# Kernel optimization log

Hardware: AMD Instinct MI355X
Metric: run time of the kernel (lower is better)

## Reference

```python
import jax, jax.numpy as jnp
import numpy as np

D_IN = 1024
D_OUT = 1024
NUM_HEADS = 16
HEAD_DIM = D_OUT // NUM_HEADS


def setup_inputs() -> dict:
    key = jax.random.key(0)
    k1, k2, k3, k4 = jax.random.split(key, 4)
    x = jax.random.normal(k1, (2, 2048, D_IN), dtype=jnp.float32)
    # Linear weights stored torch-style [out_features, in_features]
    W_qkv = jax.random.normal(k2, (3 * D_OUT, D_IN), dtype=jnp.float32) * (1.0 / np.sqrt(D_IN))
    W_out = jax.random.normal(k3, (D_OUT, D_OUT), dtype=jnp.float32) * (1.0 / np.sqrt(D_OUT))
    b_out = jax.random.normal(k4, (D_OUT,), dtype=jnp.float32) * 0.01
    return {"x": x, "W_qkv": W_qkv, "W_out": W_out, "b_out": b_out}


def reference(x, W_qkv, W_out, b_out):
    b, s, _ = x.shape
    qkv = jnp.einsum('bsi,oi->bso', x, W_qkv)  # [b, s, 3*d_out]
    q, k, v = jnp.split(qkv, 3, axis=-1)
    def to_heads(t):
        return t.reshape(b, s, NUM_HEADS, HEAD_DIM).transpose(0, 2, 1, 3)
    q, k, v = to_heads(q), to_heads(k), to_heads(v)
    # NOTE: original module does NOT scale by 1/sqrt(head_dim)
    scores = jnp.einsum('bhqd,bhkd->bhqk', q, k)
    causal = jnp.tril(jnp.ones((s, s), dtype=bool))  # True = keep
    scores = jnp.where(causal[None, None], scores, -jnp.inf)
    attn = jax.nn.softmax(scores, axis=-1)
    ctx = jnp.einsum('bhqk,bhkd->bhqd', attn, v)
    ctx = ctx.transpose(0, 2, 1, 3).reshape(b, s, D_OUT)
    return jnp.einsum('bso,po->bsp', ctx, W_out) + b_out
```

## Files before the change

kernel.cpp:

```cpp
#include <hip/hip_runtime.h>
#include <cstdint>
#include <cstddef>


typedef __attribute__((ext_vector_type(8))) short bf16x8;
typedef __attribute__((ext_vector_type(4))) float f32x4;

#define LOG2E 1.44269504f

#define MFMA16(a, b, c) __builtin_amdgcn_mfma_f32_16x16x32_bf16((a), (b), (c), 0, 0, 0)

#define GLDS16(g, s)                                                        \
  __builtin_amdgcn_global_load_lds(                                         \
      (const __attribute__((address_space(1))) void*)(g),                   \
      (__attribute__((address_space(3))) void*)(s), 16, 0, 0)

#if __has_builtin(__builtin_amdgcn_exp2f)
#define EXP2F(x) __builtin_amdgcn_exp2f(x)
#else
#define EXP2F(x) exp2f(x)
#endif

static __device__ __forceinline__ unsigned short f2bf(float f) {
  unsigned int u = __builtin_bit_cast(unsigned int, f);
  u += 0x7FFFu + ((u >> 16) & 1u);
  return (unsigned short)(u >> 16);
}

static __device__ __forceinline__ unsigned int pk2bf(float a, float b) {
  const unsigned int ua = __builtin_bit_cast(unsigned int, a) + 0x8000u;
  const unsigned int ub = __builtin_bit_cast(unsigned int, b) + 0x8000u;
  return __builtin_amdgcn_perm(ub, ua, 0x07060302);
}

__global__ __launch_bounds__(256) void cast_bf16(const float* __restrict__ x,
                                                 const float* __restrict__ wq,
                                                 const float* __restrict__ wo,
                                                 unsigned short* __restrict__ xb,
                                                 unsigned short* __restrict__ wqb,
                                                 unsigned short* __restrict__ wob)
{
  const int id = blockIdx.x * 256 + threadIdx.x;
  const float* src;
  unsigned short* dst;
  int off;
  if (id < 1048576)               { src = x;  dst = xb;  off = id; }
  else if (id < 1048576 + 786432) { src = wq; dst = wqb; off = id - 1048576; }
  else                            { src = wo; dst = wob; off = id - (1048576 + 786432); }
  float4 v = ((const float4*)src)[off];
  ushort4 o;
  o.x = f2bf(v.x); o.y = f2bf(v.y); o.z = f2bf(v.z); o.w = f2bf(v.w);
  ((ushort4*)dst)[off] = o;
}

template <int MODE>
__global__ __launch_bounds__(256) void gemm_bt(const unsigned short* __restrict__ A,
                                               const unsigned short* __restrict__ B,
                                               const float* __restrict__ bias,
                                               float* __restrict__ OutF,
                                               unsigned short* __restrict__ Qb,
                                               unsigned short* __restrict__ Kb,
                                               unsigned short* __restrict__ Vt)
{
  __shared__ unsigned short pool[16384];

  const int tid  = threadIdx.x;
  const int wave = tid >> 6, lane = tid & 63, quad = lane >> 4, cl = lane & 15;
  const int wm = wave >> 1, wn = wave & 1;
  const int m0 = blockIdx.y * 128, n0 = blockIdx.x * 128;
  const int sr = lane >> 2, sc = lane & 3;

  const int part = (MODE == 1) ? (n0 >> 10) : 0;
  const bool swapped = (MODE == 0) || (part < 2);

  f32x4 acc[4][4];
  #pragma unroll
  for (int i = 0; i < 4; ++i)
    #pragma unroll
    for (int j = 0; j < 4; ++j)
      #pragma unroll
      for (int r = 0; r < 4; ++r) acc[i][j][r] = 0.f;

  const int scs = (sc ^ ((sr >> 1) & 3)) * 8;
  const int rchunk = (quad ^ ((cl >> 1) & 3)) * 8;

  auto stage = [&](int k0, int buf) {
    unsigned short* As = pool + buf * 4096;
    unsigned short* Bs = pool + 8192 + buf * 4096;
    #pragma unroll
    for (int ii = 0; ii < 2; ++ii) {
      const int r = wave * 32 + ii * 16 + sr;
      GLDS16(A + (size_t)(m0 + r) * 1024 + k0 + scs, &As[(wave * 32 + ii * 16) * 32]);
      GLDS16(B + (size_t)(n0 + r) * 1024 + k0 + scs, &Bs[(wave * 32 + ii * 16) * 32]);
    }
  };

  stage(0, 0);
  #pragma unroll 1
  for (int it = 0; it < 32; ++it) {
    const int cur = it & 1;
    __syncthreads();
    if (it + 1 < 32) stage((it + 1) * 32, cur ^ 1);

    const unsigned short* As = pool + cur * 4096;
    const unsigned short* Bs = pool + 8192 + cur * 4096;
    bf16x8 af[4], bfr[4];
    #pragma unroll
    for (int mt = 0; mt < 4; ++mt)
      af[mt] = *(const bf16x8*)&As[(wm * 64 + mt * 16 + cl) * 32 + rchunk];
    #pragma unroll
    for (int nt = 0; nt < 4; ++nt)
      bfr[nt] = *(const bf16x8*)&Bs[(wn * 64 + nt * 16 + cl) * 32 + rchunk];

    if (swapped) {
      #pragma unroll
      for (int mt = 0; mt < 4; ++mt)
        #pragma unroll
        for (int nt = 0; nt < 4; ++nt)
          acc[mt][nt] = MFMA16(bfr[nt], af[mt], acc[mt][nt]);
    } else {
      #pragma unroll
      for (int mt = 0; mt < 4; ++mt)
        #pragma unroll
        for (int nt = 0; nt < 4; ++nt)
          acc[mt][nt] = MFMA16(af[mt], bfr[nt], acc[mt][nt]);
    }
  }

  if (MODE == 1) {
    const int bb = m0 >> 11, ss = m0 & 2047;
    if (part == 2) {
      #pragma unroll
      for (int half = 0; half < 2; ++half) {
        __syncthreads();
        if (wn == half) {
          #pragma unroll
          for (int mt = 0; mt < 4; ++mt)
            #pragma unroll
            for (int nt = 0; nt < 4; ++nt) {
              const int nl = nt * 16 + cl;
              const int ml = wm * 64 + mt * 16 + quad * 4;
              ushort4 pk;
              pk.x = f2bf(acc[mt][nt][0]); pk.y = f2bf(acc[mt][nt][1]);
              pk.z = f2bf(acc[mt][nt][2]); pk.w = f2bf(acc[mt][nt][3]);
              *(ushort4*)&pool[nl * 136 + ml] = pk;
            }
        }
        __syncthreads();
        const int row = tid >> 2, q4 = tid & 3;
        const int nglob = n0 + half * 64 + row;
        const int hh = (nglob >> 6) & 15, d = nglob & 63;
        unsigned short* drow = Vt + ((size_t)(bb * 16 + hh) * 64 + d) * 2048 + ss;
        #pragma unroll
        for (int i = 0; i < 4; ++i) {
          const bf16x8 v = *(const bf16x8*)&pool[row * 136 + q4 * 32 + i * 8];
          *(bf16x8*)(drow + q4 * 32 + i * 8) = v;
        }
      }
    } else {
      unsigned short* dst = (part == 0) ? Qb : Kb;
      const float sc2 = (part == 0) ? LOG2E : 1.0f;
      #pragma unroll
      for (int mt = 0; mt < 4; ++mt) {
        const int m = ss + wm * 64 + mt * 16 + cl;
        #pragma unroll
        for (int nt = 0; nt < 4; ++nt) {
          const int np = (n0 & 1023) + wn * 64 + nt * 16 + quad * 4;
          const int hh = np >> 6, d0 = np & 63;
          ushort4 pk;
          pk.x = f2bf(acc[mt][nt][0] * sc2);
          pk.y = f2bf(acc[mt][nt][1] * sc2);
          pk.z = f2bf(acc[mt][nt][2] * sc2);
          pk.w = f2bf(acc[mt][nt][3] * sc2);
          *(ushort4*)&dst[((size_t)(bb * 16 + hh) * 2048 + m) * 64 + d0] = pk;
        }
      }
    }
  } else {
    #pragma unroll
    for (int mt = 0; mt < 4; ++mt) {
      const int m = m0 + wm * 64 + mt * 16 + cl;
      #pragma unroll
      for (int nt = 0; nt < 4; ++nt) {
        const int n = n0 + wn * 64 + nt * 16 + quad * 4;
        const float4 bv = *(const float4*)(bias + n);
        float4 o;
        o.x = acc[mt][nt][0] + bv.x; o.y = acc[mt][nt][1] + bv.y;
        o.z = acc[mt][nt][2] + bv.z; o.w = acc[mt][nt][3] + bv.w;
        *(float4*)&OutF[(size_t)m * 1024 + n] = o;
      }
    }
  }
}

__global__ __launch_bounds__(256) void attn_mfma(const unsigned short* __restrict__ Qb,
                                                 const unsigned short* __restrict__ Kb,
                                                 const unsigned short* __restrict__ Vt,
                                                 unsigned short* __restrict__ CTX)
{
  __shared__ unsigned short Ksm[2][64 * 64];
  __shared__ unsigned short Vsm[2][64 * 64];
  __shared__ unsigned short Psm[4][32 * 40];

  const int tid  = threadIdx.x;
  const int wave = tid >> 6, lane = tid & 63, quad = lane >> 4, cl = lane & 15;

  const int L  = blockIdx.x;
  const int bh = 4 * (L & 7) + ((L >> 3) & 3);
  const int b  = bh >> 4, h = bh & 15;
  const int p  = L >> 5;
  const int g  = p * 4 + wave;
  const int qlo = g * 16;
  const int qhi = (127 - g) * 16;
  const size_t base = (size_t)bh * (2048 * 64);

  bf16x8 qf[2][2];
  #pragma unroll
  for (int dk = 0; dk < 2; ++dk) {
    qf[0][dk] = *(const bf16x8*)(Qb + base + (size_t)(qlo + cl) * 64 + dk * 32 + quad * 8);
    qf[1][dk] = *(const bf16x8*)(Qb + base + (size_t)(qhi + cl) * 64 + dk * 32 + quad * 8);
  }

  f32x4 oacc[2][4];
  #pragma unroll
  for (int mf = 0; mf < 2; ++mf)
    #pragma unroll
    for (int dt = 0; dt < 4; ++dt)
      #pragma unroll
      for (int r = 0; r < 4; ++r) oacc[mf][dt][r] = 0.f;
  float lr[2][4] = {};

  bf16x8 ones;
  #pragma unroll
  for (int k = 0; k < 8; ++k) ones[k] = (short)0x3F80;

  const int lrow  = lane >> 3;
  const int lslot = (lane & 7) ^ lrow;
  const int nch = 32 - p;

  #pragma unroll
  for (int ii = 0; ii < 2; ++ii) {
    const int r0 = wave * 16 + ii * 8;
    GLDS16(Kb + base + (size_t)(r0 + lrow) * 64 + lslot * 8, &Ksm[0][r0 * 64]);
    GLDS16(Vt + base + (size_t)(r0 + lrow) * 2048 + lslot * 8, &Vsm[0][r0 * 64]);
  }

  #pragma unroll 1
  for (int ch = 0; ch < nch; ++ch) {
    const int cur = ch & 1;
    __syncthreads();
    if (ch + 1 < nch) {
      const int j64n = (ch + 1) * 64;
      #pragma unroll
      for (int ii = 0; ii < 2; ++ii) {
        const int r0 = wave * 16 + ii * 8;
        GLDS16(Kb + base + (size_t)(j64n + r0 + lrow) * 64 + lslot * 8,
               &Ksm[cur ^ 1][r0 * 64]);
        GLDS16(Vt + base + (size_t)(r0 + lrow) * 2048 + j64n + lslot * 8,
               &Vsm[cur ^ 1][r0 * 64]);
      }
    }

    const int j64 = ch * 64;
    #pragma unroll
    for (int jli = 0; jli < 2; ++jli) {
      const int jg0 = j64 + jli * 32;
      if (jg0 > qhi + 15) continue;
      const bool lowAct = (jg0 <= qlo + 15);
      const int jl = jli * 32;

      bf16x8 kf[2][2];
      #pragma unroll
      for (int jf = 0; jf < 2; ++jf)
        #pragma unroll
        for (int dk = 0; dk < 2; ++dk) {
          const int jrow = jl + jf * 16 + cl;
          const int slot = (dk * 4 + quad) ^ (cl & 7);
          kf[jf][dk] = *(const bf16x8*)&Ksm[cur][jrow * 64 + slot * 8];
        }

      f32x4 st[2][2];
      #pragma unroll
      for (int jf = 0; jf < 2; ++jf)
        #pragma unroll
        for (int mf = 0; mf < 2; ++mf) {
          if (mf == 0 && !lowAct) continue;
          f32x4 z;
          #pragma unroll
          for (int r = 0; r < 4; ++r) z[r] = 0.f;
          z = MFMA16(kf[jf][0], qf[mf][0], z);
          st[jf][mf] = MFMA16(kf[jf][1], qf[mf][1], z);
        }

      #pragma unroll
      for (int mf = 0; mf < 2; ++mf) {
        if (mf == 0 && !lowAct) continue;
        const int qbase = mf ? qhi : qlo;
        const bool diag = (jg0 + 32 > qbase);
        #pragma unroll
        for (int jf = 0; jf < 2; ++jf) {
          float pv[4];
          if (diag) {
            const int qg = qbase + cl;
            #pragma unroll
            for (int r = 0; r < 4; ++r) {
              const int jg = jg0 + jf * 16 + quad * 4 + r;
              pv[r] = (jg <= qg) ? EXP2F(st[jf][mf][r]) : 0.f;
            }
          } else {
            #pragma unroll
            for (int r = 0; r < 4; ++r) pv[r] = EXP2F(st[jf][mf][r]);
          }
          uint2 w;
          w.x = pk2bf(pv[0], pv[1]);
          w.y = pk2bf(pv[2], pv[3]);
          *(uint2*)&Psm[wave][(mf * 16 + cl) * 40 + jf * 16 + quad * 4] = w;
        }
      }

      bf16x8 vf[4];
      #pragma unroll
      for (int dt = 0; dt < 4; ++dt) {
        const int d = dt * 16 + cl;
        const int slot = ((jl >> 3) + quad) ^ (cl & 7);
        vf[dt] = *(const bf16x8*)&Vsm[cur][d * 64 + slot * 8];
      }

      #pragma unroll
      for (int mf = 0; mf < 2; ++mf) {
        if (mf == 0 && !lowAct) continue;
        const bf16x8 pf = *(const bf16x8*)&Psm[wave][(mf * 16 + cl) * 40 + quad * 8];
        f32x4 z;
        #pragma unroll
        for (int r = 0; r < 4; ++r) z[r] = 0.f;
        const f32x4 ls = MFMA16(pf, ones, z);
        #pragma unroll
        for (int r = 0; r < 4; ++r) lr[mf][r] += ls[r];
        #pragma unroll
        for (int dt = 0; dt < 4; ++dt)
          oacc[mf][dt] = MFMA16(pf, vf[dt], oacc[mf][dt]);
      }
    }
  }

  #pragma unroll
  for (int mf = 0; mf < 2; ++mf) {
    const int qbase = mf ? qhi : qlo;
    float inv[4];
    #pragma unroll
    for (int r = 0; r < 4; ++r) inv[r] = 1.f / lr[mf][r];
    #pragma unroll
    for (int dt = 0; dt < 4; ++dt)
      #pragma unroll
      for (int r = 0; r < 4; ++r)
        CTX[(size_t)(b * 2048 + qbase + quad * 4 + r) * 1024 +
            h * 64 + dt * 16 + cl] = f2bf(oacc[mf][dt][r] * inv[r]);
  }
}

extern "C" void kernel_launch(void* const* d_in, const int* in_sizes, int n_in,
                              void* d_out, int out_size, void* d_ws, size_t ws_size,
                              hipStream_t stream)
{
  const float* x    = (const float*)d_in[0];
  const float* Wqkv = (const float*)d_in[1];
  const float* Wout = (const float*)d_in[2];
  const float* bout = (const float*)d_in[3];
  float* out = (float*)d_out;

  char* ws = (char*)d_ws;
  unsigned short* xb  = (unsigned short*)(ws);
  unsigned short* wqb = (unsigned short*)(ws + 8388608);
  unsigned short* wob = (unsigned short*)(ws + 14680064);
  unsigned short* Qb  = (unsigned short*)(ws + 16777216);
  unsigned short* Kb  = (unsigned short*)(ws + 25165824);
  unsigned short* Vt  = (unsigned short*)(ws + 33554432);
  unsigned short* CTX = (unsigned short*)(ws + 41943040);

  cast_bf16<<<dim3(8192), dim3(256), 0, stream>>>(x, Wqkv, Wout, xb, wqb, wob);

  gemm_bt<1><<<dim3(24, 32), dim3(256), 0, stream>>>(xb, wqb, nullptr, nullptr, Qb, Kb, Vt);

  attn_mfma<<<dim3(512), dim3(256), 0, stream>>>(Qb, Kb, Vt, CTX);

  gemm_bt<0><<<dim3(8, 32), dim3(256), 0, stream>>>(CTX, wob, bout, out, nullptr, nullptr, nullptr);
}
```

Measured before the change: 202.6 us.

## Triple-buffer GEMM and attention K staging with vmcnt-based barriers

The GEMM main loop moves from double to triple LDS buffering, prefetching two K-steps ahead. It replaces __syncthreads with a barrier that waits only until the oldest stage's global-to-LDS loads land (s_waitcnt vmcnt(N)), so one barrier per iteration is enough. The attention kernel triple-buffers only K in LDS the same way, and now loads V fragments straight from global memory into registers instead of staging them through LDS. The aim is more overlap of memory latency with MFMA work and less LDS traffic, at the cost of extra LDS in the GEMM and uncoalesced-ish direct V loads whose latency is now exposed inside each chunk.

```diff
diff --git a/kernel.cpp b/kernel.cpp
--- a/kernel.cpp
+++ b/kernel.cpp
@@ -14,6 +14,8 @@
   __builtin_amdgcn_global_load_lds(                                         \
       (const __attribute__((address_space(1))) void*)(g),                   \
       (__attribute__((address_space(3))) void*)(s), 16, 0, 0)
+
+#define ASYNC_BAR(N) asm volatile("s_waitcnt vmcnt(" #N ")\n\ts_barrier" ::: "memory")
 
 #if __has_builtin(__builtin_amdgcn_exp2f)
 #define EXP2F(x) __builtin_amdgcn_exp2f(x)
@@ -62,7 +64,7 @@
                                                unsigned short* __restrict__ Kb,
                                                unsigned short* __restrict__ Vt)
 {
-  __shared__ unsigned short pool[16384];
+  __shared__ unsigned short pool[24576];
 
   const int tid  = threadIdx.x;
   const int wave = tid >> 6, lane = tid & 63, quad = lane >> 4, cl = lane & 15;
@@ -85,8 +87,8 @@
   const int rchunk = (quad ^ ((cl >> 1) & 3)) * 8;
 
   auto stage = [&](int k0, int buf) {
-    unsigned short* As = pool + buf * 4096;
-    unsigned short* Bs = pool + 8192 + buf * 4096;
+    unsigned short* As = pool + buf * 8192;
+    unsigned short* Bs = As + 4096;
     #pragma unroll
     for (int ii = 0; ii < 2; ++ii) {
       const int r = wave * 32 + ii * 16 + sr;
@@ -96,14 +98,22 @@
   };
 
   stage(0, 0);
+  stage(32, 1);
+  int cur = 0;
   #pragma unroll 1
   for (int it = 0; it < 32; ++it) {
-    const int cur = it & 1;
-    __syncthreads();
-    if (it + 1 < 32) stage((it + 1) * 32, cur ^ 1);
-
-    const unsigned short* As = pool + cur * 4096;
-    const unsigned short* Bs = pool + 8192 + cur * 4096;
+    if (it + 2 < 32) {
+      ASYNC_BAR(4);
+      const int bnx = (cur == 0) ? 2 : cur - 1;
+      stage((it + 2) * 32, bnx);
+    } else if (it + 1 < 32) {
+      ASYNC_BAR(4);
+    } else {
+      ASYNC_BAR(0);
+    }
+
+    const unsigned short* As = pool + cur * 8192;
+    const unsigned short* Bs = As + 4096;
     bf16x8 af[4], bfr[4];
     #pragma unroll
     for (int mt = 0; mt < 4; ++mt)
@@ -125,6 +135,7 @@
         for (int nt = 0; nt < 4; ++nt)
           acc[mt][nt] = MFMA16(af[mt], bfr[nt], acc[mt][nt]);
     }
+    cur = (cur == 2) ? 0 : cur + 1;
   }
 
   if (MODE == 1) {
@@ -198,8 +209,7 @@
                                                  const unsigned short* __restrict__ Vt,
                                                  unsigned short* __restrict__ CTX)
 {
-  __shared__ unsigned short Ksm[2][64 * 64];
-  __shared__ unsigned short Vsm[2][64 * 64];
+  __shared__ unsigned short Ksm[3][64 * 64];
   __shared__ unsigned short Psm[4][32 * 40];
 
   const int tid  = threadIdx.x;
@@ -213,6 +223,7 @@
   const int qlo = g * 16;
   const int qhi = (127 - g) * 16;
   const size_t base = (size_t)bh * (2048 * 64);
+  const unsigned short* Vp = Vt + base;
 
   bf16x8 qf[2][2];
   #pragma unroll
@@ -238,27 +249,27 @@
   const int lslot = (lane & 7) ^ lrow;
   const int nch = 32 - p;
 
-  #pragma unroll
-  for (int ii = 0; ii < 2; ++ii) {
-    const int r0 = wave * 16 + ii * 8;
-    GLDS16(Kb + base + (size_t)(r0 + lrow) * 64 + lslot * 8, &Ksm[0][r0 * 64]);
-    GLDS16(Vt + base + (size_t)(r0 + lrow) * 2048 + lslot * 8, &Vsm[0][r0 * 64]);
-  }
-
+  auto stageK = [&](int j64, int buf) {
+    #pragma unroll
+    for (int ii = 0; ii < 2; ++ii) {
+      const int r0 = wave * 16 + ii * 8;
+      GLDS16(Kb + base + (size_t)(j64 + r0 + lrow) * 64 + lslot * 8, &Ksm[buf][r0 * 64]);
+    }
+  };
+
+  stageK(0, 0);
+  stageK(64, 1);
+  int cur = 0;
   #pragma unroll 1
   for (int ch = 0; ch < nch; ++ch) {
-    const int cur = ch & 1;
-    __syncthreads();
-    if (ch + 1 < nch) {
-      const int j64n = (ch + 1) * 64;
-      #pragma unroll
-      for (int ii = 0; ii < 2; ++ii) {
-        const int r0 = wave * 16 + ii * 8;
-        GLDS16(Kb + base + (size_t)(j64n + r0 + lrow) * 64 + lslot * 8,
-               &Ksm[cur ^ 1][r0 * 64]);
-        GLDS16(Vt + base + (size_t)(r0 + lrow) * 2048 + j64n + lslot * 8,
-               &Vsm[cur ^ 1][r0 * 64]);
-      }
+    if (ch + 2 < nch) {
+      ASYNC_BAR(2);
+      const int bnx = (cur == 0) ? 2 : cur - 1;
+      stageK((ch + 2) * 64, bnx);
+    } else if (ch + 1 < nch) {
+      ASYNC_BAR(2);
+    } else {
+      ASYNC_BAR(0);
     }
 
     const int j64 = ch * 64;
@@ -268,6 +279,11 @@
       if (jg0 > qhi + 15) continue;
       const bool lowAct = (jg0 <= qlo + 15);
       const int jl = jli * 32;
+
+      bf16x8 vf[4];
+      #pragma unroll
+      for (int dt = 0; dt < 4; ++dt)
+        vf[dt] = *(const bf16x8*)(Vp + (size_t)(dt * 16 + cl) * 2048 + jg0 + quad * 8);
 
       bf16x8 kf[2][2];
       #pragma unroll
@@ -318,14 +334,6 @@
         }
       }
 
-      bf16x8 vf[4];
-      #pragma unroll
-      for (int dt = 0; dt < 4; ++dt) {
-        const int d = dt * 16 + cl;
-        const int slot = ((jl >> 3) + quad) ^ (cl & 7);
-        vf[dt] = *(const bf16x8*)&Vsm[cur][d * 64 + slot * 8];
-      }
-
       #pragma unroll
       for (int mf = 0; mf < 2; ++mf) {
         if (mf == 0 && !lowAct) continue;
@@ -341,6 +349,7 @@
           oacc[mf][dt] = MFMA16(pf, vf[dt], oacc[mf][dt]);
       }
     }
+    cur = (cur == 2) ? 0 : cur + 1;
   }
 
   #pragma unroll
```

Result: slower. 219.6 us (+8.4%).
